# Kernel optimization log

Hardware: AMD Instinct MI355X
Metric: run time of the kernel (lower is better)

## Reference

```python
import jax, jax.numpy as jnp
import numpy as np

B, L, D_MODEL = 8, 1024, 512
D_STATE, D_CONV, EXPAND = 16, 4, 2
D_INNER = EXPAND * D_MODEL          # 1024
DT_RANK = (D_MODEL + 15) // 16      # 32
D_FF = 4 * D_MODEL                  # 2048
EPS = 1e-12


def setup_inputs() -> dict:
    key = jax.random.key(0)
    ks = jax.random.split(key, 16)
    s = 0.02
    n = lambda k, shp: jax.random.normal(k, shp, dtype=jnp.float32) * s
    A = jnp.tile(jnp.arange(1, D_STATE + 1, dtype=jnp.float32)[None, :], (D_INNER, 1))
    return {
        "x": jax.random.normal(ks[0], (B, L, D_MODEL), dtype=jnp.float32),
        "in_proj_w": n(ks[1], (2 * D_INNER, D_MODEL)),
        "conv_w": n(ks[2], (D_INNER, 1, D_CONV)),
        "conv_b": jnp.zeros((D_INNER,), jnp.float32),
        "x_proj_w": n(ks[3], (DT_RANK + 2 * D_STATE, D_INNER)),
        "dt_proj_w": n(ks[4], (D_INNER, DT_RANK)),
        "dt_proj_b": jnp.full((D_INNER,), -4.0, jnp.float32),  # softplus(~-4) -> small dt
        "A_log": jnp.log(A),
        "D": jnp.ones((D_INNER,), jnp.float32),
        "out_proj_w": n(ks[5], (D_MODEL, D_INNER)),
        "ln1_g": jnp.ones((D_MODEL,), jnp.float32),
        "ln1_b": jnp.zeros((D_MODEL,), jnp.float32),
        "fc1_w": n(ks[6], (D_FF, D_MODEL)),
        "fc1_b": jnp.zeros((D_FF,), jnp.float32),
        "fc2_w": n(ks[7], (D_MODEL, D_FF)),
        "fc2_b": jnp.zeros((D_MODEL,), jnp.float32),
        "ln2_g": jnp.ones((D_MODEL,), jnp.float32),
        "ln2_b": jnp.zeros((D_MODEL,), jnp.float32),
    }


def _layernorm(x, g, b):
    m = jnp.mean(x, axis=-1, keepdims=True)
    v = jnp.var(x, axis=-1, keepdims=True)
    return (x - m) * jax.lax.rsqrt(v + EPS) * g + b


def _mamba(x, in_proj_w, conv_w, conv_b, x_proj_w, dt_proj_w, dt_proj_b, A_log, D, out_proj_w):
    # in_proj: [B,L,d_model] -> [B,L,2*d_inner]
    xz = jnp.einsum("bld,ed->ble", x, in_proj_w)
    u, z = jnp.split(xz, 2, axis=-1)                      # each [B,L,d_inner]
    # depthwise causal conv over time
    uc = jax.lax.conv_general_dilated(
        jnp.transpose(u, (0, 2, 1)), conv_w,
        window_strides=(1,), padding=[(D_CONV - 1, 0)],
        feature_group_count=D_INNER,
        dimension_numbers=("NCH", "OIH", "NCH"))
    u = jnp.transpose(uc, (0, 2, 1)) + conv_b             # [B,L,d_inner]
    u = jax.nn.silu(u)
    # x_proj -> dt, B, C
    x_dbl = jnp.einsum("bld,ed->ble", u, x_proj_w)
    dt, Bm, Cm = jnp.split(x_dbl, [DT_RANK, DT_RANK + D_STATE], axis=-1)
    dt = jax.nn.softplus(jnp.einsum("blr,dr->bld", dt, dt_proj_w) + dt_proj_b)  # [B,L,d_inner]
    A = -jnp.exp(A_log)                                   # [d_inner, d_state]
    deltaA = jnp.exp(dt[..., None] * A)                   # [B,L,d_inner,d_state]
    deltaBu = dt[..., None] * Bm[:, :, None, :] * u[..., None]

    def step(h, inp):
        dA_t, dBu_t, C_t = inp                            # [B,di,ds],[B,di,ds],[B,ds]
        h = h * dA_t + dBu_t
        y = jnp.einsum("bds,bs->bd", h, C_t)
        return h, y

    h0 = jnp.zeros((x.shape[0], D_INNER, D_STATE), x.dtype)
    _, ys = jax.lax.scan(step, h0, (jnp.transpose(deltaA, (1, 0, 2, 3)),
                                    jnp.transpose(deltaBu, (1, 0, 2, 3)),
                                    jnp.transpose(Cm, (1, 0, 2))))
    y = jnp.transpose(ys, (1, 0, 2)) + u * D              # [B,L,d_inner]
    y = y * jax.nn.silu(z)
    return jnp.einsum("ble,de->bld", y, out_proj_w)


def reference(x, in_proj_w, conv_w, conv_b, x_proj_w, dt_proj_w, dt_proj_b, A_log, D,
              out_proj_w, ln1_g, ln1_b, fc1_w, fc1_b, fc2_w, fc2_b, ln2_g, ln2_b):
    h = _mamba(x, in_proj_w, conv_w, conv_b, x_proj_w, dt_proj_w, dt_proj_b,
               A_log, D, out_proj_w)
    h = _layernorm(h + x, ln1_g, ln1_b)                   # dropout = identity (eval)
    # FeedForward with residual + LayerNorm
    f = jax.nn.gelu(jnp.einsum("bld,fd->blf", h, fc1_w) + fc1_b, approximate=False)
    f = jnp.einsum("blf,df->bld", f, fc2_w) + fc2_b
    return _layernorm(f + h, ln2_g, ln2_b)
```

## Files before the change

### kernel.cpp

```cpp
#include <hip/hip_runtime.h>
#include <hip/hip_bf16.h>
#include <math.h>

typedef __hip_bfloat16 bf16;
typedef unsigned short u16;
typedef unsigned int u32;
typedef __attribute__((ext_vector_type(8))) short short8;
typedef __attribute__((ext_vector_type(4))) float f32x4;
typedef __attribute__((ext_vector_type(4))) u32 u32x4;

#define B_  8
#define L_  1024
#define DM  512
#define DI  1024
#define DS  16
#define DR  32
#define DF  2048
#define M_  (B_ * L_)

__device__ __forceinline__ float b2f(bf16 x) { return __bfloat162float(x); }
__device__ __forceinline__ bf16  f2b(float x) { return __float2bfloat16(x); }
__device__ __forceinline__ u16   bu(bf16 x)  { return __builtin_bit_cast(u16, x); }
__device__ __forceinline__ float s2f(short x) { return b2f(__builtin_bit_cast(bf16, (u16)x)); }
__device__ __forceinline__ float uphi(u32 w) { return __builtin_bit_cast(float, w & 0xffff0000u); }
__device__ __forceinline__ float uplo(u32 w) { return __builtin_bit_cast(float, w << 16); }

__device__ __forceinline__ bool is_b16(const void* flag) {
    return ((const u16*)flag)[0] == 0x3F80;
}
__device__ __forceinline__ float ldr(const void* p, size_t i, bool b16) {
    return b16 ? b2f(((const bf16*)p)[i]) : ((const float*)p)[i];
}

__device__ __forceinline__ float fexp2(float x) {
#if __has_builtin(__builtin_amdgcn_exp2f)
    return __builtin_amdgcn_exp2f(x);
#else
    return __expf(x * 0.6931471805599453f);
#endif
}

__device__ __forceinline__ void gload16(const bf16* g, bf16* l) {
    __builtin_amdgcn_global_load_lds(
        (const __attribute__((address_space(1))) unsigned int*)g,
        (__attribute__((address_space(3))) unsigned int*)l, 16, 0, 0);
}

__device__ __forceinline__ float fsilu(float x) {
    return x * __builtin_amdgcn_rcpf(1.f + __expf(-x));
}

#define CN0 (M_ * DM)
#define CN1 (CN0 + 2 * DI * DM)
#define CN2 (CN1 + 64 * DI)
#define CN3 (CN2 + DI * DR)
#define CN4 (CN3 + DM * DI)
#define CN5 (CN4 + DF * DM)
#define CN6 (CN5 + DM * DF)
#define CN7 (CN6 + DI * 4)
#define CN8 (CN7 + DI)
#define CN9 (CN8 + DI)
__global__ __launch_bounds__(256) void cvt_all_kernel(
    const void* s0, const void* s1, const void* s2, const void* s3,
    const void* s4, const void* s5, const void* s6, const void* s7,
    const void* s8, const void* s9,
    bf16* __restrict__ dst, const void* __restrict__ flag)
{
    const bool b16 = is_b16(flag);
    const long i = ((long)blockIdx.x * 256 + threadIdx.x) * 8;
    if (i >= CN9) return;
    const void* src; long off;
    if      (i < CN0) { src = s0; off = i; }
    else if (i < CN1) { src = s1; off = i - CN0; }
    else if (i < CN2) { src = s2; off = i - CN1; }
    else if (i < CN3) { src = s3; off = i - CN2; }
    else if (i < CN4) { src = s4; off = i - CN3; }
    else if (i < CN5) { src = s5; off = i - CN4; }
    else if (i < CN6) { src = s6; off = i - CN5; }
    else if (i < CN7) { src = s7; off = i - CN6; }
    else if (i < CN8) { src = s8; off = i - CN7; }
    else              { src = s9; off = i - CN8; }
    if (b16) {
        *(short8*)(dst + i) = *(const short8*)((const bf16*)src + off);
    } else {
        const float* f = (const float*)src + off;
        const f32x4 a = *(const f32x4*)f;
        const f32x4 b = *(const f32x4*)(f + 4);
        short8 o;
#pragma unroll
        for (int k = 0; k < 4; ++k) {
            o[k]     = (short)bu(f2b(a[k]));
            o[k + 4] = (short)bu(f2b(b[k]));
        }
        *(short8*)(dst + i) = o;
    }
}

template <int BM, int BN, int NT, int ACT, int PACK>
__global__ __launch_bounds__(NT) void mfma_gemm(
    const bf16* __restrict__ A, int lda,
    const bf16* __restrict__ W, int ldw,
    const void* __restrict__ bias,
    bf16* __restrict__ C, int ldc,
    int K, const void* __restrict__ flag,
    void* __restrict__ pk, void* __restrict__ pk2,
    const bf16* __restrict__ uin)
{
    constexpr int WN = (BN >= 128) ? 2 : 1;
    constexpr int CA = BM * 4 / NT;
    constexpr int CB = BN * 4 / NT;
    constexpr int BUF = (BM + BN) * 32;
    __shared__ __align__(16) bf16 smem[2 * BUF];
    const int tid  = threadIdx.x;
    const int wave = tid >> 6, lane = tid & 63;
    const int quad = lane >> 4, l16 = lane & 15;
    const u32 gx  = gridDim.x;
    const u32 nwg = gx * gridDim.y;
    const u32 lid = blockIdx.y * gx + blockIdx.x;
    const u32 swz = (lid & 7) * (nwg >> 3) + (lid >> 3);
    const int bm = (int)(swz / gx) * BM, bn = (int)(swz % gx) * BN;
    const int wm = (wave / WN) * 64, wn = (wave % WN) * 64;

    f32x4 acc[4][4];
#pragma unroll
    for (int i = 0; i < 4; ++i)
#pragma unroll
        for (int j = 0; j < 4; ++j) acc[i][j] = (f32x4){0.f, 0.f, 0.f, 0.f};

    auto load_tile = [&](int k0, int p) {
        bf16* As = smem + p * BUF;
        bf16* Ws = As + BM * 32;
#pragma unroll
        for (int j = 0; j < CA; ++j) {
            const int e = j * NT + tid;
            gload16(A + (size_t)(bm + (e >> 2)) * lda + k0 + (e & 3) * 8, As + e * 8);
        }
#pragma unroll
        for (int j = 0; j < CB; ++j) {
            const int e = j * NT + tid;
            gload16(W + (size_t)(bn + (e >> 2)) * ldw + k0 + (e & 3) * 8, Ws + e * 8);
        }
    };

    const int NIT = K >> 5;
    load_tile(0, 0);
    for (int it = 0; it < NIT; ++it) {
        __syncthreads();
        if (it + 1 < NIT) load_tile((it + 1) << 5, (it + 1) & 1);
        const bf16* As = smem + (it & 1) * BUF;
        const bf16* Ws = As + BM * 32;
        short8 af[4], wf[4];
#pragma unroll
        for (int mt = 0; mt < 4; ++mt)
            af[mt] = *(const short8*)(As + (wm + mt * 16 + l16) * 32 + quad * 8);
#pragma unroll
        for (int nt = 0; nt < 4; ++nt)
            wf[nt] = *(const short8*)(Ws + (wn + nt * 16 + l16) * 32 + quad * 8);
#pragma unroll
        for (int mt = 0; mt < 4; ++mt)
#pragma unroll
            for (int nt = 0; nt < 4; ++nt)
                acc[mt][nt] = __builtin_amdgcn_mfma_f32_16x16x32_bf16(
                    af[mt], wf[nt], acc[mt][nt], 0, 0, 0);
    }

    const bool b16 = bias ? is_b16(flag) : false;
#pragma unroll
    for (int nt = 0; nt < 4; ++nt) {
        const int col = bn + wn + nt * 16 + l16;
        const float bv = bias ? ldr(bias, col, b16) : 0.f;
#pragma unroll
        for (int mt = 0; mt < 4; ++mt)
#pragma unroll
            for (int i = 0; i < 4; ++i) {
                const int row = bm + wm + mt * 16 + quad * 4 + i;
                float v = acc[mt][nt][i] + bv;
                if (ACT == 1) v = (v > 20.f) ? v : log1pf(__expf(v));
                else if (ACT == 2)
                    v = 0.5f * v * (1.f + erff(v * 0.7071067811865475f));
                if (PACK == 1) {
                    const float uv = b2f(uin[(size_t)row * ldc + col]);
                    ((float*)pk)[(size_t)row * ldc + col]  = v;
                    ((float*)pk2)[(size_t)row * ldc + col] = v * uv;
                } else {
                    C[(size_t)row * ldc + col] = f2b(v);
                }
            }
    }
    if (PACK == 2) {
#pragma unroll
        for (int mt = 0; mt < 4; ++mt)
#pragma unroll
            for (int i = 0; i < 4; ++i) {
                const int row = bm + wm + mt * 16 + quad * 4 + i;
                ((float*)pk)[(size_t)row * 16 + l16]  = acc[mt][2][i];
                ((float*)pk2)[(size_t)row * 16 + l16] = acc[mt][3][i];
            }
    }
}

__global__ __launch_bounds__(256) void conv_silu_kernel(
    const bf16* __restrict__ xz,
    const bf16* __restrict__ cw,
    const bf16* __restrict__ cb,
    const bf16* __restrict__ Dw,
    bf16* __restrict__ u,
    u32* __restrict__ ug)
{
    const int t  = blockIdx.x * 256 + threadIdx.x;
    const long t8 = (long)t * 8;
    const int d8  = (int)(t8 & (DI - 1));
    const int row = (int)(t8 >> 10);
    const int l   = row & (L_ - 1);

    short8 wraw[4];
#pragma unroll
    for (int k = 0; k < 4; ++k)
        wraw[k] = *(const short8*)(cw + (size_t)d8 * 4 + k * 8);
    const short8 cbv = *(const short8*)(cb + d8);
    const short8 dv  = *(const short8*)(Dw + d8);

    float acc[8];
#pragma unroll
    for (int i = 0; i < 8; ++i) acc[i] = s2f(cbv[i]);
#pragma unroll
    for (int j = 0; j < 4; ++j) {
        const int ls = l - 3 + j;
        if (ls >= 0) {
            const short8 xv = *(const short8*)(xz + (size_t)(row - 3 + j) * (2 * DI) + d8);
#pragma unroll
            for (int i = 0; i < 8; ++i) {
                const int f = i * 4 + j;
                acc[i] += s2f(wraw[f >> 3][f & 7]) * s2f(xv[i]);
            }
        }
    }
    const short8 zv = *(const short8*)(xz + (size_t)row * (2 * DI) + DI + d8);
    short8 us;
    u32x4 g0, g1;
#pragma unroll
    for (int i = 0; i < 8; ++i) {
        const float uv = fsilu(acc[i]);
        us[i] = (short)bu(f2b(uv));
        const float gz = fsilu(s2f(zv[i]));
        const float g2 = uv * s2f(dv[i]) * gz;
        const u32 p = ((u32)bu(f2b(g2)) << 16) | bu(f2b(gz));
        if (i < 4) g0[i] = p; else g1[i - 4] = p;
    }
    *(short8*)(u + t8) = us;
    *(u32x4*)(ug + t8) = g0;
    *(u32x4*)(ug + t8 + 4) = g1;
}

__global__ __launch_bounds__(256) void scan_kernel(
    const float* __restrict__ dtf,
    const float* __restrict__ duf,
    const float* __restrict__ Bf,
    const float* __restrict__ Cf,
    const u32* __restrict__ ug,
    const void* __restrict__ A_log,
    bf16* __restrict__ y,
    const void* __restrict__ flag)
{
    const bool b16 = is_b16(flag);
    const int tid = threadIdx.x;
    const int lane = tid & 63;
    const int s  = lane & 15;
    const int dl = tid >> 4;
    const int b = blockIdx.x >> 6, dch = blockIdx.x & 63;
    const int d0 = dch * 16, d = d0 + dl;
    const float AcL = -__expf(ldr(A_log, (size_t)d * DS + s, b16))
                      * 1.4426950408889634f;

    __shared__ __align__(16) float dt_s[16][68];
    __shared__ __align__(16) float du_s[16][68];
    __shared__ __align__(16) float B_s[16][68];
    __shared__ __align__(16) float C_s[16][68];
    __shared__ u32 ug_s[16][68];
    __shared__ bf16 y_s[16][72];
    __shared__ float p_s[16][16][33];

    const int c16 = tid & 15, r16 = tid >> 4;
    float rdt[4], rdu[4], rB[4], rC[4];
    u32 rug[4];
    const size_t base = (size_t)b * L_;

    auto load_chunk = [&](int l0) {
#pragma unroll
        for (int j = 0; j < 4; ++j) {
            const size_t row = base + l0 + r16 + 16 * j;
            rdt[j] = dtf[row * DI + d0 + c16];
            rdu[j] = duf[row * DI + d0 + c16];
            rug[j] = ug[row * DI + d0 + c16];
            rB[j]  = Bf[row * 16 + c16];
            rC[j]  = Cf[row * 16 + c16];
        }
    };
    auto store_chunk = [&]() {
#pragma unroll
        for (int j = 0; j < 4; ++j) {
            dt_s[c16][r16 + 16 * j] = rdt[j];
            du_s[c16][r16 + 16 * j] = rdu[j];
            ug_s[c16][r16 + 16 * j] = rug[j];
            B_s[c16][r16 + 16 * j]  = rB[j];
            C_s[c16][r16 + 16 * j]  = rC[j];
        }
    };

    float h = 0.f;
    float* const prow = &p_s[dl][s][0];
    load_chunk(0);
    for (int c = 0; c < 16; ++c) {
        store_chunk();
        __syncthreads();
        if (c < 15) load_chunk((c + 1) * 64);
#pragma unroll
        for (int g = 0; g < 2; ++g) {
#pragma unroll
            for (int w2 = 0; w2 < 2; ++w2) {
                const int w = g * 2 + w2;
                f32x4 dtw[4], duw[4], bw[4], cw[4];
#pragma unroll
                for (int q = 0; q < 4; ++q) {
                    dtw[q] = *(const f32x4*)&dt_s[dl][w * 16 + q * 4];
                    duw[q] = *(const f32x4*)&du_s[dl][w * 16 + q * 4];
                    bw[q]  = *(const f32x4*)&B_s[s][w * 16 + q * 4];
                    cw[q]  = *(const f32x4*)&C_s[s][w * 16 + q * 4];
                }
#pragma unroll
                for (int t = 0; t < 16; ++t) {
                    const float e = fexp2(dtw[t >> 2][t & 3] * AcL);
                    h = fmaf(h, e, duw[t >> 2][t & 3] * bw[t >> 2][t & 3]);
                    prow[w2 * 16 + t] = h * cw[t >> 2][t & 3];
                }
            }
            asm volatile("s_waitcnt lgkmcnt(0)" ::: "memory");
#pragma unroll
            for (int w2 = 0; w2 < 2; ++w2) {
                const int w = g * 2 + w2;
                const u32 ugw = ug_s[dl][w * 16 + s];
                float pr[16];
#pragma unroll
                for (int k = 0; k < 16; ++k) pr[k] = p_s[dl][k][w2 * 16 + s];
#pragma unroll
                for (int o = 8; o >= 1; o >>= 1)
#pragma unroll
                    for (int i = 0; i < o; ++i) pr[i] += pr[i + o];
                y_s[dl][w * 16 + s] = f2b(fmaf(pr[0], uplo(ugw), uphi(ugw)));
            }
        }
        __syncthreads();
#pragma unroll
        for (int j = 0; j < 4; ++j) {
            const size_t row = base + c * 64 + r16 + 16 * j;
            y[row * DI + d0 + c16] = y_s[c16][r16 + 16 * j];
        }
    }
}

template <int RMODE, int OMODE>
__global__ __launch_bounds__(256) void ln_kernel(
    const bf16* __restrict__ inp,
    const bf16* __restrict__ res,
    const void* __restrict__ g,
    const void* __restrict__ bb,
    void* __restrict__ out,
    const void* __restrict__ flag)
{
    const bool b16 = is_b16(flag);
    const int wv = threadIdx.x >> 6, lane = threadIdx.x & 63;
    const int row = blockIdx.x * 4 + wv;
    const size_t off = (size_t)row * DM;
    const int e = lane * 8;

    float v[8];
    const short8 iv = *(const short8*)(inp + off + e);
    const short8 rv = *(const short8*)(res + off + e);
#pragma unroll
    for (int i = 0; i < 8; ++i) v[i] = s2f(iv[i]) + s2f(rv[i]);

    float sum = 0.f, sq = 0.f;
#pragma unroll
    for (int i = 0; i < 8; ++i) { sum += v[i]; sq += v[i] * v[i]; }
#pragma unroll
    for (int o = 32; o >= 1; o >>= 1) {
        sum += __shfl_xor(sum, o);
        sq  += __shfl_xor(sq, o);
    }
    const float m = sum * (1.f / DM);
    const float var = sq * (1.f / DM) - m * m;
    const float inv = rsqrtf(fmaxf(var, 0.f) + 1e-12f);

    float gv[8], bv[8];
    if (b16) {
        const short8 gg = *(const short8*)((const bf16*)g + e);
        const short8 bg = *(const short8*)((const bf16*)bb + e);
#pragma unroll
        for (int i = 0; i < 8; ++i) { gv[i] = s2f(gg[i]); bv[i] = s2f(bg[i]); }
    } else {
        const float* gf = (const float*)g + e;
        const float* bf = (const float*)bb + e;
        const f32x4 g0 = *(const f32x4*)gf, g1 = *(const f32x4*)(gf + 4);
        const f32x4 b0 = *(const f32x4*)bf, b1 = *(const f32x4*)(bf + 4);
#pragma unroll
        for (int i = 0; i < 8; ++i) {
            gv[i] = i < 4 ? g0[i] : g1[i - 4];
            bv[i] = i < 4 ? b0[i] : b1[i - 4];
        }
    }
    float o[8];
#pragma unroll
    for (int i = 0; i < 8; ++i) o[i] = (v[i] - m) * inv * gv[i] + bv[i];

    if (OMODE == 2 && !b16) {
        f32x4 o0, o1;
#pragma unroll
        for (int i = 0; i < 4; ++i) { o0[i] = o[i]; o1[i] = o[i + 4]; }
        *(f32x4*)((float*)out + off + e) = o0;
        *(f32x4*)((float*)out + off + e + 4) = o1;
    } else {
        short8 os;
#pragma unroll
        for (int i = 0; i < 8; ++i) os[i] = (short)bu(f2b(o[i]));
        *(short8*)((bf16*)out + off + e) = os;
    }
}

extern "C" void kernel_launch(void* const* d_in, const int* in_sizes, int n_in,
                              void* d_out, int out_size, void* d_ws, size_t ws_size,
                              hipStream_t stream)
{
    (void)in_sizes; (void)n_in; (void)out_size; (void)ws_size;
    const void* x       = d_in[0];
    const void* in_w    = d_in[1];
    const void* conv_w  = d_in[2];
    const void* conv_b  = d_in[3];
    const void* xproj_w = d_in[4];
    const void* dt_w    = d_in[5];
    const void* dt_b    = d_in[6];
    const void* A_log   = d_in[7];
    const void* Dw      = d_in[8];
    const void* out_w   = d_in[9];
    const void* ln1_g   = d_in[10];
    const void* ln1_b   = d_in[11];
    const void* fc1_w   = d_in[12];
    const void* fc1_b   = d_in[13];
    const void* fc2_w   = d_in[14];
    const void* fc2_b   = d_in[15];
    const void* ln2_g   = d_in[16];
    const void* ln2_b   = d_in[17];
    const void* flag    = ln1_g;

    bf16* xb    = (bf16*)d_ws;
    bf16* inwb  = xb    + (size_t)M_ * DM;
    bf16* xpwb  = inwb  + (size_t)2 * DI * DM;
    bf16* dtwb  = xpwb  + (size_t)64 * DI;
    bf16* outwb = dtwb  + (size_t)DI * DR;
    bf16* fc1wb = outwb + (size_t)DM * DI;
    bf16* fc2wb = fc1wb + (size_t)DF * DM;
    bf16* cwb   = fc2wb + (size_t)DM * DF;
    bf16* cbb   = cwb   + (size_t)DI * 4;
    bf16* dwb   = cbb   + (size_t)DI;
    bf16* xz    = dwb   + (size_t)DI;
    bf16* u     = xz    + (size_t)M_ * 2 * DI;
    bf16* xdbl  = u     + (size_t)M_ * DI;
    float* dtf  = (float*)(xdbl + (size_t)M_ * 64);
    u32*  ugp   = (u32*)(dtf + (size_t)M_ * DI);
    float* Bfp  = (float*)(ugp + (size_t)M_ * DI);
    bf16* yb    = (bf16*)(Bfp + (size_t)M_ * 16);
    bf16* hb    = yb    + (size_t)M_ * DI;
    float* duf  = (float*)xz;
    float* Cfp  = (float*)hb;
    bf16* mo    = (bf16*)dtf;
    bf16* fb    = xz;
    bf16* f2b_  = yb;

    dim3 blk(256);
    cvt_all_kernel<<<dim3((CN9 / 8 + 255) / 256), blk, 0, stream>>>(
        x, in_w, xproj_w, dt_w, out_w, fc1_w, fc2_w, conv_w, conv_b, Dw,
        xb, flag);

    mfma_gemm<128, 128, 256, 0, 0><<<dim3(16, 64), blk, 0, stream>>>(
        xb, DM, inwb, DM, nullptr, xz, 2 * DI, DM, flag, nullptr, nullptr, nullptr);
    conv_silu_kernel<<<dim3(M_ * DI / 8 / 256), blk, 0, stream>>>(
        xz, cwb, cbb, dwb, u, ugp);
    mfma_gemm<128, 64, 128, 0, 2><<<dim3(1, 64), dim3(128), 0, stream>>>(
        u, DI, xpwb, DI, nullptr, xdbl, 64, DI, flag, Bfp, Cfp, nullptr);
    mfma_gemm<128, 128, 256, 1, 1><<<dim3(8, 64), blk, 0, stream>>>(
        xdbl, 64, dtwb, DR, dt_b, nullptr, DI, DR, flag, dtf, duf, u);
    scan_kernel<<<dim3(B_ * 64), blk, 0, stream>>>(
        dtf, duf, Bfp, Cfp, ugp, A_log, yb, flag);
    mfma_gemm<128, 128, 256, 0, 0><<<dim3(4, 64), blk, 0, stream>>>(
        yb, DI, outwb, DI, nullptr, mo, DM, DI, flag, nullptr, nullptr, nullptr);
    ln_kernel<1, 1><<<dim3(M_ / 4), blk, 0, stream>>>(
        mo, xb, ln1_g, ln1_b, hb, flag);
    mfma_gemm<128, 128, 256, 2, 0><<<dim3(16, 64), blk, 0, stream>>>(
        hb, DM, fc1wb, DM, fc1_b, fb, DF, DM, flag, nullptr, nullptr, nullptr);
    mfma_gemm<128, 128, 256, 0, 0><<<dim3(4, 64), blk, 0, stream>>>(
        fb, DF, fc2wb, DF, fc2_b, f2b_, DM, DF, flag, nullptr, nullptr, nullptr);
    ln_kernel<1, 2><<<dim3(M_ / 4), blk, 0, stream>>>(
        f2b_, hb, ln2_g, ln2_b, d_out, flag);
}
```

Measured before the change: 397.4 us.

## Split selective scan into time segments with carry-fix pass; retile narrow GEMMs

The sequential scan over 1024 timesteps is cut into four 256-step segments, each run in parallel from a zero state. Each segment records its final state and cumulative decay product. A second kernel then adds the carried-in state's contribution (decayed prefix times C, gated) to the outputs of segments 1 to 3. This raises the scan's block count from 512 to 2048, at the cost of an extra pass that rereads dt, C, gate and y. Separately, the out_proj and fc2 GEMMs switch to a 128x64 tile so they launch more blocks.

```diff
diff --git a/kernel.cpp b/kernel.cpp
--- a/kernel.cpp
+++ b/kernel.cpp
@@ -17,6 +17,8 @@
 #define DR  32
 #define DF  2048
 #define M_  (B_ * L_)
+#define SEG  4
+#define SEGT 256
 
 __device__ __forceinline__ float b2f(bf16 x) { return __bfloat162float(x); }
 __device__ __forceinline__ bf16  f2b(float x) { return __float2bfloat16(x); }
@@ -252,13 +254,118 @@
     *(u32x4*)(ug + t8 + 4) = g1;
 }
 
-__global__ __launch_bounds__(256) void scan_kernel(
+__global__ __launch_bounds__(256) void scan_seg_kernel(
     const float* __restrict__ dtf,
     const float* __restrict__ duf,
     const float* __restrict__ Bf,
     const float* __restrict__ Cf,
     const u32* __restrict__ ug,
     const void* __restrict__ A_log,
+    bf16* __restrict__ y,
+    float* __restrict__ hseg,
+    float* __restrict__ Pseg,
+    const void* __restrict__ flag)
+{
+    const bool b16 = is_b16(flag);
+    const int tid = threadIdx.x;
+    const int lane = tid & 63;
+    const int s  = lane & 15;
+    const int dl = tid >> 4;
+    const int bx = blockIdx.x;
+    const int seg = bx >> 9, b = (bx >> 6) & 7, dch = bx & 63;
+    const int d0 = dch * 16, d = d0 + dl;
+    const float AcL = -__expf(ldr(A_log, (size_t)d * DS + s, b16))
+                      * 1.4426950408889634f;
+
+    __shared__ __align__(16) float dt_s[16][36];
+    __shared__ __align__(16) float du_s[16][36];
+    __shared__ __align__(16) float B_s[16][36];
+    __shared__ __align__(16) float C_s[16][36];
+    __shared__ u32 ug_s[16][36];
+    __shared__ bf16 y_s[16][36];
+    __shared__ float p_s[16][16][17];
+
+    const int c16 = tid & 15, r16 = tid >> 4;
+    float rdt[2], rdu[2], rB[2], rC[2];
+    u32 rug[2];
+    const size_t base = (size_t)b * L_ + (size_t)seg * SEGT;
+
+    auto load_chunk = [&](int l0) {
+#pragma unroll
+        for (int j = 0; j < 2; ++j) {
+            const size_t row = base + l0 + r16 + 16 * j;
+            rdt[j] = dtf[row * DI + d0 + c16];
+            rdu[j] = duf[row * DI + d0 + c16];
+            rug[j] = ug[row * DI + d0 + c16];
+            rB[j]  = Bf[row * 16 + c16];
+            rC[j]  = Cf[row * 16 + c16];
+        }
+    };
+    auto store_chunk = [&]() {
+#pragma unroll
+        for (int j = 0; j < 2; ++j) {
+            dt_s[c16][r16 + 16 * j] = rdt[j];
+            du_s[c16][r16 + 16 * j] = rdu[j];
+            ug_s[c16][r16 + 16 * j] = rug[j];
+            B_s[c16][r16 + 16 * j]  = rB[j];
+            C_s[c16][r16 + 16 * j]  = rC[j];
+        }
+    };
+
+    float h = 0.f, P = 1.f;
+    float* const prow = &p_s[dl][s][0];
+    load_chunk(0);
+    for (int c = 0; c < 8; ++c) {
+        store_chunk();
+        __syncthreads();
+        if (c < 7) load_chunk((c + 1) * 32);
+#pragma unroll
+        for (int w = 0; w < 2; ++w) {
+            f32x4 dtw[4], duw[4], bw[4], cw[4];
+#pragma unroll
+            for (int q = 0; q < 4; ++q) {
+                dtw[q] = *(const f32x4*)&dt_s[dl][w * 16 + q * 4];
+                duw[q] = *(const f32x4*)&du_s[dl][w * 16 + q * 4];
+                bw[q]  = *(const f32x4*)&B_s[s][w * 16 + q * 4];
+                cw[q]  = *(const f32x4*)&C_s[s][w * 16 + q * 4];
+            }
+            const u32 ugw = ug_s[dl][w * 16 + s];
+#pragma unroll
+            for (int t = 0; t < 16; ++t) {
+                const float e = fexp2(dtw[t >> 2][t & 3] * AcL);
+                P *= e;
+                h = fmaf(h, e, duw[t >> 2][t & 3] * bw[t >> 2][t & 3]);
+                prow[t] = h * cw[t >> 2][t & 3];
+            }
+            asm volatile("s_waitcnt lgkmcnt(0)" ::: "memory");
+            float pr[16];
+#pragma unroll
+            for (int k = 0; k < 16; ++k) pr[k] = p_s[dl][k][s];
+#pragma unroll
+            for (int o = 8; o >= 1; o >>= 1)
+#pragma unroll
+                for (int i = 0; i < o; ++i) pr[i] += pr[i + o];
+            y_s[dl][w * 16 + s] = f2b(fmaf(pr[0], uplo(ugw), uphi(ugw)));
+        }
+        __syncthreads();
+#pragma unroll
+        for (int j = 0; j < 2; ++j) {
+            const size_t row = base + c * 32 + r16 + 16 * j;
+            y[row * DI + d0 + c16] = y_s[c16][r16 + 16 * j];
+        }
+    }
+    const size_t hidx = (((size_t)seg * B_ + b) * DI + d) * DS + s;
+    hseg[hidx] = h;
+    Pseg[hidx] = P;
+}
+
+__global__ __launch_bounds__(256) void scan_fix_kernel(
+    const float* __restrict__ dtf,
+    const float* __restrict__ Cf,
+    const u32* __restrict__ ug,
+    const void* __restrict__ A_log,
+    const float* __restrict__ hseg,
+    const float* __restrict__ Pseg,
     bf16* __restrict__ y,
     const void* __restrict__ flag)
 {
@@ -267,93 +374,90 @@
     const int lane = tid & 63;
     const int s  = lane & 15;
     const int dl = tid >> 4;
-    const int b = blockIdx.x >> 6, dch = blockIdx.x & 63;
+    const int bx = blockIdx.x;
+    const int seg = 1 + (bx >> 9), b = (bx >> 6) & 7, dch = bx & 63;
     const int d0 = dch * 16, d = d0 + dl;
     const float AcL = -__expf(ldr(A_log, (size_t)d * DS + s, b16))
                       * 1.4426950408889634f;
 
-    __shared__ __align__(16) float dt_s[16][68];
-    __shared__ __align__(16) float du_s[16][68];
-    __shared__ __align__(16) float B_s[16][68];
-    __shared__ __align__(16) float C_s[16][68];
-    __shared__ u32 ug_s[16][68];
-    __shared__ bf16 y_s[16][72];
-    __shared__ float p_s[16][16][33];
+    const size_t hb0 = ((size_t)b * DI + d) * DS + s;
+    const size_t segstride = (size_t)B_ * DI * DS;
+    float hc = hseg[hb0];
+    for (int m = 1; m < seg; ++m)
+        hc = fmaf(Pseg[hb0 + (size_t)m * segstride], hc,
+                  hseg[hb0 + (size_t)m * segstride]);
+
+    __shared__ __align__(16) float dt_s[16][36];
+    __shared__ __align__(16) float C_s[16][36];
+    __shared__ u32 ug_s[16][36];
+    __shared__ u16 y2_s[2][16][36];
+    __shared__ float p_s[16][16][17];
 
     const int c16 = tid & 15, r16 = tid >> 4;
-    float rdt[4], rdu[4], rB[4], rC[4];
-    u32 rug[4];
-    const size_t base = (size_t)b * L_;
+    float rdt[2], rC[2];
+    u32 rug[2];
+    u16 ry[2];
+    const size_t base = (size_t)b * L_ + (size_t)seg * SEGT;
 
     auto load_chunk = [&](int l0) {
 #pragma unroll
-        for (int j = 0; j < 4; ++j) {
+        for (int j = 0; j < 2; ++j) {
             const size_t row = base + l0 + r16 + 16 * j;
             rdt[j] = dtf[row * DI + d0 + c16];
-            rdu[j] = duf[row * DI + d0 + c16];
             rug[j] = ug[row * DI + d0 + c16];
-            rB[j]  = Bf[row * 16 + c16];
             rC[j]  = Cf[row * 16 + c16];
+            ry[j]  = ((const u16*)y)[row * DI + d0 + c16];
         }
     };
-    auto store_chunk = [&]() {
-#pragma unroll
-        for (int j = 0; j < 4; ++j) {
+    auto store_chunk = [&](int par) {
+#pragma unroll
+        for (int j = 0; j < 2; ++j) {
             dt_s[c16][r16 + 16 * j] = rdt[j];
-            du_s[c16][r16 + 16 * j] = rdu[j];
             ug_s[c16][r16 + 16 * j] = rug[j];
-            B_s[c16][r16 + 16 * j]  = rB[j];
             C_s[c16][r16 + 16 * j]  = rC[j];
+            y2_s[par][c16][r16 + 16 * j] = ry[j];
         }
     };
 
-    float h = 0.f;
+    float Q = hc;
     float* const prow = &p_s[dl][s][0];
     load_chunk(0);
-    for (int c = 0; c < 16; ++c) {
-        store_chunk();
+    for (int c = 0; c < 8; ++c) {
+        const int par = c & 1;
+        store_chunk(par);
         __syncthreads();
-        if (c < 15) load_chunk((c + 1) * 64);
-#pragma unroll
-        for (int g = 0; g < 2; ++g) {
-#pragma unroll
-            for (int w2 = 0; w2 < 2; ++w2) {
-                const int w = g * 2 + w2;
-                f32x4 dtw[4], duw[4], bw[4], cw[4];
-#pragma unroll
-                for (int q = 0; q < 4; ++q) {
-                    dtw[q] = *(const f32x4*)&dt_s[dl][w * 16 + q * 4];
-                    duw[q] = *(const f32x4*)&du_s[dl][w * 16 + q * 4];
-                    bw[q]  = *(const f32x4*)&B_s[s][w * 16 + q * 4];
-                    cw[q]  = *(const f32x4*)&C_s[s][w * 16 + q * 4];
-                }
-#pragma unroll
-                for (int t = 0; t < 16; ++t) {
-                    const float e = fexp2(dtw[t >> 2][t & 3] * AcL);
-                    h = fmaf(h, e, duw[t >> 2][t & 3] * bw[t >> 2][t & 3]);
-                    prow[w2 * 16 + t] = h * cw[t >> 2][t & 3];
-                }
+        if (c < 7) load_chunk((c + 1) * 32);
+#pragma unroll
+        for (int w = 0; w < 2; ++w) {
+            f32x4 dtw[4], cw[4];
+#pragma unroll
+            for (int q = 0; q < 4; ++q) {
+                dtw[q] = *(const f32x4*)&dt_s[dl][w * 16 + q * 4];
+                cw[q]  = *(const f32x4*)&C_s[s][w * 16 + q * 4];
+            }
+            const u32 ugw = ug_s[dl][w * 16 + s];
+#pragma unroll
+            for (int t = 0; t < 16; ++t) {
+                Q *= fexp2(dtw[t >> 2][t & 3] * AcL);
+                prow[t] = Q * cw[t >> 2][t & 3];
             }
             asm volatile("s_waitcnt lgkmcnt(0)" ::: "memory");
-#pragma unroll
-            for (int w2 = 0; w2 < 2; ++w2) {
-                const int w = g * 2 + w2;
-                const u32 ugw = ug_s[dl][w * 16 + s];
-                float pr[16];
-#pragma unroll
-                for (int k = 0; k < 16; ++k) pr[k] = p_s[dl][k][w2 * 16 + s];
-#pragma unroll
-                for (int o = 8; o >= 1; o >>= 1)
-#pragma unroll
-                    for (int i = 0; i < o; ++i) pr[i] += pr[i + o];
-                y_s[dl][w * 16 + s] = f2b(fmaf(pr[0], uplo(ugw), uphi(ugw)));
-            }
+            float pr[16];
+#pragma unroll
+            for (int k = 0; k < 16; ++k) pr[k] = p_s[dl][k][s];
+#pragma unroll
+            for (int o = 8; o >= 1; o >>= 1)
+#pragma unroll
+                for (int i = 0; i < o; ++i) pr[i] += pr[i + o];
+            const float old = s2f((short)y2_s[par][dl][w * 16 + s]);
+            y2_s[par][dl][w * 16 + s] =
+                bu(f2b(fmaf(pr[0], uplo(ugw), old)));
         }
         __syncthreads();
 #pragma unroll
-        for (int j = 0; j < 4; ++j) {
-            const size_t row = base + c * 64 + r16 + 16 * j;
-            y[row * DI + d0 + c16] = y_s[c16][r16 + 16 * j];
+        for (int j = 0; j < 2; ++j) {
+            const size_t row = base + c * 32 + r16 + 16 * j;
+            ((u16*)y)[row * DI + d0 + c16] = y2_s[par][c16][r16 + 16 * j];
         }
     }
 }
@@ -471,6 +575,8 @@
     bf16* hb    = yb    + (size_t)M_ * DI;
     float* duf  = (float*)xz;
     float* Cfp  = (float*)hb;
+    float* hseg = (float*)u;
+    float* Pseg = hseg + (size_t)SEG * B_ * DI * DS;
     bf16* mo    = (bf16*)dtf;
     bf16* fb    = xz;
     bf16* f2b_  = yb;
@@ -488,15 +594,17 @@
         u, DI, xpwb, DI, nullptr, xdbl, 64, DI, flag, Bfp, Cfp, nullptr);
     mfma_gemm<128, 128, 256, 1, 1><<<dim3(8, 64), blk, 0, stream>>>(
         xdbl, 64, dtwb, DR, dt_b, nullptr, DI, DR, flag, dtf, duf, u);
-    scan_kernel<<<dim3(B_ * 64), blk, 0, stream>>>(
-        dtf, duf, Bfp, Cfp, ugp, A_log, yb, flag);
-    mfma_gemm<128, 128, 256, 0, 0><<<dim3(4, 64), blk, 0, stream>>>(
+    scan_seg_kernel<<<dim3(B_ * 64 * SEG), blk, 0, stream>>>(
+        dtf, duf, Bfp, Cfp, ugp, A_log, yb, hseg, Pseg, flag);
+    scan_fix_kernel<<<dim3(B_ * 64 * (SEG - 1)), blk, 0, stream>>>(
+        dtf, Cfp, ugp, A_log, hseg, Pseg, yb, flag);
+    mfma_gemm<128, 64, 128, 0, 0><<<dim3(8, 64), dim3(128), 0, stream>>>(
         yb, DI, outwb, DI, nullptr, mo, DM, DI, flag, nullptr, nullptr, nullptr);
     ln_kernel<1, 1><<<dim3(M_ / 4), blk, 0, stream>>>(
         mo, xb, ln1_g, ln1_b, hb, flag);
     mfma_gemm<128, 128, 256, 2, 0><<<dim3(16, 64), blk, 0, stream>>>(
         hb, DM, fc1wb, DM, fc1_b, fb, DF, DM, flag, nullptr, nullptr, nullptr);
-    mfma_gemm<128, 128, 256, 0, 0><<<dim3(4, 64), blk, 0, stream>>>(
+    mfma_gemm<128, 64, 128, 0, 0><<<dim3(8, 64), dim3(128), 0, stream>>>(
         fb, DF, fc2wb, DF, fc2_b, f2b_, DM, DF, flag, nullptr, nullptr, nullptr);
     ln_kernel<1, 2><<<dim3(M_ / 4), blk, 0, stream>>>(
         f2b_, hb, ln2_g, ln2_b, d_out, flag);
```

Measured after the change: 419.6 us. +5.6%, slower.
